# Kernel tuning notes

Measured on AMD Instinct MI355X. Metric: run time of the kernel, lower is better.

The kernel has to match this reference:

```python
import jax, jax.numpy as jnp
import numpy as np

B, N, L = 2, 512, 8
DIM, HEADS, DIM_HEAD, NBRS = 64, 8, 128, 30
INNER = HEADS * DIM_HEAD


def _ln(x, g, b):
    mu = x.mean(-1, keepdims=True)
    v = ((x - mu) ** 2).mean(-1, keepdims=True)
    return (x - mu) * jax.lax.rsqrt(v + 1e-5) * g + b


def _gather_rows(t, idx):
    # t: (n, ...) rows gathered per batch; t (b,n,...), idx (b,i,j) -> (b,i,j,...)
    return jax.vmap(lambda tb, ib: tb[ib])(t, idx)


def _en_layer(h, coors, edges, mask, lp):
    (ln1_g, ln1_b, qkv_w, out_w, out_b, ew1, eb1, ew2, eb2,
     cw1, cb1, cw2, cb2, c_scale, c_comb, ln2_g, ln2_b,
     fw1, fb1, fw2, fb2) = lp
    b, n, _ = h.shape
    x = _ln(h, ln1_g, ln1_b)
    q, k, v = jnp.split(x @ qkv_w, 3, axis=-1)
    q = q.reshape(b, n, HEADS, DIM_HEAD)
    k = k.reshape(b, n, HEADS, DIM_HEAD)
    v = v.reshape(b, n, HEADS, DIM_HEAD)

    rel = coors[:, :, None, :] - coors[:, None, :, :]          # (b,n,n,3)
    dist2 = (rel * rel).sum(-1)                                 # squared dist, same ordering as norm
    pair_ok = mask[:, :, None] & mask[:, None, :]
    ranking = jnp.where(pair_ok, jax.lax.stop_gradient(dist2), 1e10)
    _, idx = jax.lax.top_k(-ranking, NBRS)                      # (b,n,nn) nearest (incl. self)

    kg = _gather_rows(k, idx)                                   # (b,n,nn,h,d)
    vg = _gather_rows(v, idx)
    rel_g = jnp.take_along_axis(rel, idx[..., None], axis=2)    # (b,n,nn,3)
    edg_g = jnp.take_along_axis(edges, idx[..., None], axis=2)  # (b,n,nn,1)
    mask_j = jnp.take_along_axis(jnp.broadcast_to(mask[:, None, :], (b, n, n)), idx, axis=2)
    valid = mask[:, :, None] & mask_j                           # (b,n,nn)

    qk = jnp.einsum('bihd,bijhd->bijh', q, kg) * (DIM_HEAD ** -0.5)
    # edge MLP conditions attention logits on pairwise edge features
    qk = jax.nn.gelu(jnp.concatenate([qk, edg_g], -1) @ ew1 + eb1) @ ew2 + eb2

    # equivariant coordinate update branch
    cw = jax.nn.gelu(jax.nn.gelu(qk) @ cw1 + cb1) @ cw2 + cb2   # (b,n,nn,h)
    cw = jnp.where(valid[..., None], cw, 0.)
    s = (rel_g * rel_g).sum(-1, keepdims=True)
    rel_n = rel_g / jnp.maximum(jnp.sqrt(jnp.where(s == 0., 1., s)), 1e-8) * c_scale
    coors = coors + jnp.einsum('bijh,bijc,h->bic', cw, rel_n, c_comb)

    # node feature attention over the 30 neighbors
    sim = jnp.where(valid[..., None], qk, -1e9)
    attn = jax.nn.softmax(sim, axis=2)
    out = jnp.einsum('bijh,bijhd->bihd', attn, vg).reshape(b, n, INNER)
    h = h + out @ out_w + out_b

    y = _ln(h, ln2_g, ln2_b)
    h = h + jax.nn.gelu(y @ fw1 + fb1) @ fw2 + fb2
    return h, coors


def _forward(mask, feats, coors, edges, fe_w, fe_b, ln1_g, ln1_b, qkv_w, out_w, out_b,
             ew1, eb1, ew2, eb2, cw1, cb1, cw2, cb2, c_scale, c_comb,
             ln2_g, ln2_b, fw1, fb1, fw2, fb2, cls_w, cls_b):
    x = jnp.concatenate([jnp.sin(feats), jnp.cos(feats)], -1)   # (b,n,6)
    h = jax.nn.relu(x @ fe_w + fe_b)                            # (b,n,64)
    lps = (ln1_g, ln1_b, qkv_w, out_w, out_b, ew1, eb1, ew2, eb2,
           cw1, cb1, cw2, cb2, c_scale, c_comb, ln2_g, ln2_b, fw1, fb1, fw2, fb2)

    def step(carry, lp):
        return _en_layer(carry[0], carry[1], edges, mask, lp), None

    (h, _), _ = jax.lax.scan(step, (h, coors), lps)
    return jax.nn.softmax(h @ cls_w + cls_b, axis=2)            # (b,n,20)


def setup_inputs() -> dict:
    key = jax.random.key(0)
    ks = jax.random.split(key, 16)
    r = lambda i, s, sc=0.02: jax.random.normal(ks[i], s, jnp.float32) * sc
    E2 = 2 * (HEADS + 1)
    return dict(
        feats=r(0, (B, N, 3), 1.0),
        coors=r(1, (B, N, 3), 3.0),
        edges=r(2, (B, N, N, 1), 1.0),
        mask=jnp.ones((B, N), dtype=bool),
        fe_w=r(3, (6, DIM)), fe_b=jnp.zeros((DIM,)),
        ln1_g=jnp.ones((L, DIM)), ln1_b=jnp.zeros((L, DIM)),
        qkv_w=r(4, (L, DIM, 3 * INNER)),
        out_w=r(5, (L, INNER, DIM)), out_b=jnp.zeros((L, DIM)),
        ew1=r(6, (L, HEADS + 1, E2), 0.1), eb1=jnp.zeros((L, E2)),
        ew2=r(7, (L, E2, HEADS), 0.1), eb2=jnp.zeros((L, HEADS)),
        cw1=r(8, (L, HEADS, 64), 0.1), cb1=jnp.zeros((L, 64)),
        cw2=r(9, (L, 64, HEADS), 0.1), cb2=jnp.zeros((L, HEADS)),
        c_scale=jnp.ones((L,)),
        c_comb=r(10, (L, HEADS), 0.1),
        ln2_g=jnp.ones((L, DIM)), ln2_b=jnp.zeros((L, DIM)),
        fw1=r(11, (L, DIM, 4 * DIM)), fb1=jnp.zeros((L, 4 * DIM)),
        fw2=r(12, (L, 4 * DIM, DIM)), fb2=jnp.zeros((L, DIM)),
        cls_w=r(13, (DIM, 20)), cls_b=jnp.zeros((20,)),
    )


def reference(feats, coors, edges, mask, fe_w, fe_b, ln1_g, ln1_b, qkv_w, out_w, out_b,
              ew1, eb1, ew2, eb2, cw1, cb1, cw2, cb2, c_scale, c_comb,
              ln2_g, ln2_b, fw1, fb1, fw2, fb2, cls_w, cls_b):
    return _forward(mask, feats, coors, edges, fe_w, fe_b, ln1_g, ln1_b, qkv_w, out_w, out_b,
                    ew1, eb1, ew2, eb2, cw1, cb1, cw2, cb2, c_scale, c_comb,
                    ln2_g, ln2_b, fw1, fb1, fw2, fb2, cls_w, cls_b)
```

## Files before the change

kernel.cpp:

```cpp
#include <hip/hip_runtime.h>
#include <hip/hip_bf16.h>

#define NV    512
#define BN    1024
#define NNB   30
#define DIM   64
#define HEADS 8
#define DH    128
#define INNER 1024

__device__ __forceinline__ float gelu_t(float x){
    float x3 = x*x*x;
    return 0.5f*x*(1.0f + tanhf(0.7978845608028654f*(x + 0.044715f*x3)));
}
__device__ __forceinline__ unsigned short f2bf(float x){
    __hip_bfloat16 h = __float2bfloat16(x);
    return __builtin_bit_cast(unsigned short, h);
}
__device__ __forceinline__ float bflo(unsigned u){ return __uint_as_float(u << 16); }
__device__ __forceinline__ float bfhi(unsigned u){ return __uint_as_float(u & 0xffff0000u); }

__global__ __launch_bounds__(256) void k_head(const float* __restrict__ h,
                                              const float* __restrict__ g,
                                              const float* __restrict__ be,
                                              const float* __restrict__ w,
                                              float* __restrict__ qf,
                                              unsigned short* __restrict__ kvh,
                                              const float* __restrict__ coors,
                                              int* __restrict__ idx,
                                              const float* __restrict__ feats,
                                              const float* __restrict__ fe_w,
                                              const float* __restrict__ fe_b,
                                              float* __restrict__ hout){
    __shared__ float At[64][68];
    __shared__ float Wt[64][132];
    int t = threadIdx.x;
    int wv = t >> 6, lane = t & 63;

    if (blockIdx.x < 384){
        int rt = blockIdx.x / 24, ct = blockIdx.x % 24;
        int row0 = rt*64, col0 = ct*128;

        float gk = g[lane], bk = be[lane];
        if (feats){
            float fb = fe_b[lane];
            float w0 = fe_w[0*DIM+lane], w1 = fe_w[1*DIM+lane], w2 = fe_w[2*DIM+lane];
            float w3 = fe_w[3*DIM+lane], w4 = fe_w[4*DIM+lane], w5 = fe_w[5*DIM+lane];
            #pragma unroll 4
            for (int rr = 0; rr < 16; rr++){
                int r = wv*16 + rr;
                int row = row0 + r;
                float f0 = feats[row*3+0], f1 = feats[row*3+1], f2 = feats[row*3+2];
                float hv = fb;
                hv += sinf(f0)*w0; hv += sinf(f1)*w1; hv += sinf(f2)*w2;
                hv += cosf(f0)*w3; hv += cosf(f1)*w4; hv += cosf(f2)*w5;
                hv = fmaxf(hv, 0.0f);
                if (ct == 0) hout[(size_t)row*DIM + lane] = hv;
                float s = hv;
                #pragma unroll
                for (int m = 32; m >= 1; m >>= 1) s += __shfl_xor(s, m, 64);
                float mu = s*(1.0f/64.0f);
                float d = hv - mu;
                float vv = d*d;
                #pragma unroll
                for (int m = 32; m >= 1; m >>= 1) vv += __shfl_xor(vv, m, 64);
                At[lane][r] = d / sqrtf(vv*(1.0f/64.0f) + 1e-5f) * gk + bk;
            }
        } else {
            #pragma unroll 4
            for (int rr = 0; rr < 16; rr++){
                int r = wv*16 + rr;
                float v = h[(row0+r)*DIM + lane];
                float s = v;
                #pragma unroll
                for (int m = 32; m >= 1; m >>= 1) s += __shfl_xor(s, m, 64);
                float mu = s*(1.0f/64.0f);
                float d = v - mu;
                float vv = d*d;
                #pragma unroll
                for (int m = 32; m >= 1; m >>= 1) vv += __shfl_xor(vv, m, 64);
                At[lane][r] = d / sqrtf(vv*(1.0f/64.0f) + 1e-5f) * gk + bk;
            }
        }
        const float* wg = w + col0;
        #pragma unroll
        for (int i = t*4; i < 64*128; i += 1024){
            int k = i >> 7, c = i & 127;
            *(float4*)&Wt[k][c] = *(const float4*)&wg[k*3072 + c];
        }
        __syncthreads();

        int ty = t >> 4, tx = t & 15;
        float acc[4][8];
        #pragma unroll
        for (int i = 0; i < 4; i++)
            #pragma unroll
            for (int j = 0; j < 8; j++) acc[i][j] = 0.0f;

        #pragma unroll 2
        for (int k = 0; k < 64; k++){
            float4 a  = *(const float4*)&At[k][ty*4];
            float4 w0 = *(const float4*)&Wt[k][tx*4];
            float4 w1 = *(const float4*)&Wt[k][64 + tx*4];
            float av[4]  = {a.x, a.y, a.z, a.w};
            float wv8[8] = {w0.x, w0.y, w0.z, w0.w, w1.x, w1.y, w1.z, w1.w};
            #pragma unroll
            for (int i = 0; i < 4; i++)
                #pragma unroll
                for (int j = 0; j < 8; j++) acc[i][j] += av[i]*wv8[j];
        }

        if (ct < 8){
            #pragma unroll
            for (int i = 0; i < 4; i++){
                int r = row0 + ty*4 + i;
                float* dst = &qf[(size_t)r*INNER + col0];
                *(float4*)&dst[tx*4]      = make_float4(acc[i][0], acc[i][1], acc[i][2], acc[i][3]);
                *(float4*)&dst[64 + tx*4] = make_float4(acc[i][4], acc[i][5], acc[i][6], acc[i][7]);
            }
        } else {
            int kvcol0 = col0 - 1024;
            #pragma unroll
            for (int i = 0; i < 4; i++){
                int r = row0 + ty*4 + i;
                unsigned short* dst = &kvh[(size_t)r*2048 + kvcol0];
                ushort4 p0 = { f2bf(acc[i][0]), f2bf(acc[i][1]), f2bf(acc[i][2]), f2bf(acc[i][3]) };
                ushort4 p1 = { f2bf(acc[i][4]), f2bf(acc[i][5]), f2bf(acc[i][6]), f2bf(acc[i][7]) };
                *(ushort4*)&dst[tx*4]      = p0;
                *(ushort4*)&dst[64 + tx*4] = p1;
            }
        }
    } else {
        int row = (blockIdx.x - 384)*4 + wv;
        int b = row >> 9;
        const float* cbp = coors + (size_t)b*NV*3;
        float cx = coors[row*3+0], cy = coors[row*3+1], cz = coors[row*3+2];
        float d2[8];
        int jb = lane*8;
        #pragma unroll
        for (int u = 0; u < 8; u++){
            float dx = cx - cbp[(jb+u)*3+0];
            float dy = cy - cbp[(jb+u)*3+1];
            float dz = cz - cbp[(jb+u)*3+2];
            d2[u] = dx*dx + dy*dy + dz*dz;
        }
        for (int sel = 0; sel < NNB; sel++){
            float bv = d2[0]; int bu = 0;
            #pragma unroll
            for (int u = 1; u < 8; u++) if (d2[u] < bv){ bv = d2[u]; bu = u; }
            int bj = jb + bu;
            #pragma unroll
            for (int m = 32; m >= 1; m >>= 1){
                float ov = __shfl_xor(bv, m, 64);
                int   oj = __shfl_xor(bj, m, 64);
                if (ov < bv || (ov == bv && oj < bj)){ bv = ov; bj = oj; }
            }
            if (lane == 0) idx[row*NNB + sel] = bj;
            #pragma unroll
            for (int u = 0; u < 8; u++) if (jb + u == bj) d2[u] = 1e30f;
        }
    }
}

__global__ __launch_bounds__(256) void k_layer(const float* __restrict__ qf,
                                               const unsigned short* __restrict__ kvh,
                                               const int*   __restrict__ idx,
                                               const float* __restrict__ cin,
                                               float*       __restrict__ cout,
                                               const float* __restrict__ edges,
                                               float* __restrict__ h,
                                               const float* __restrict__ ew1, const float* __restrict__ eb1,
                                               const float* __restrict__ ew2, const float* __restrict__ eb2,
                                               const float* __restrict__ cw1, const float* __restrict__ cb1,
                                               const float* __restrict__ cw2, const float* __restrict__ cb2,
                                               const float* __restrict__ c_scale, const float* __restrict__ c_comb,
                                               const float* __restrict__ out_w,  const float* __restrict__ out_b,
                                               const float* __restrict__ g2, const float* __restrict__ b2,
                                               const float* __restrict__ fw1, const float* __restrict__ fb1,
                                               const float* __restrict__ fw2, const float* __restrict__ fb2,
                                               const float* __restrict__ cls_w, const float* __restrict__ cls_b,
                                               float* __restrict__ cls_out){
    int row = blockIdx.x;
    int b = row >> 9, i = row & (NV-1);
    int t = threadIdx.x;
    int wave = t >> 6, lane = t & 63;

    __shared__ float qk[NNB][HEADS];
    __shared__ float lg[NNB][HEADS];
    __shared__ float t18[NNB][18];
    __shared__ float t64s[NNB][65];
    __shared__ float cwh[NNB][HEADS];
    __shared__ float attn[NNB][HEADS];
    __shared__ float ej[NNB];
    __shared__ float reln[NNB][3];
    __shared__ float wj[NNB];
    __shared__ int   jid[NNB];
    __shared__ float As[INNER];
    __shared__ float red[256];
    __shared__ float hsr[DIM];
    __shared__ float ys[DIM];
    __shared__ float us[256];

    if (t < NNB) jid[t] = idx[row*NNB + t];
    __syncthreads();

    float qreg[16];
    {
        const float4* qp = (const float4*)&qf[(size_t)row*INNER + lane*16];
        #pragma unroll
        for (int e = 0; e < 4; e++){
            float4 v = qp[e];
            qreg[e*4+0] = v.x; qreg[e*4+1] = v.y; qreg[e*4+2] = v.z; qreg[e*4+3] = v.w;
        }
    }

    if (t < NNB){
        int jj = jid[t];
        ej[t] = edges[(size_t)(b*NV+i)*NV + jj];
        float rx = cin[(b*NV+i)*3+0] - cin[(b*NV+jj)*3+0];
        float ry = cin[(b*NV+i)*3+1] - cin[(b*NV+jj)*3+1];
        float rz = cin[(b*NV+i)*3+2] - cin[(b*NV+jj)*3+2];
        float s = rx*rx + ry*ry + rz*rz;
        float den = fmaxf(sqrtf(s == 0.0f ? 1.0f : s), 1e-8f);
        float cs = c_scale[0];
        reln[t][0] = rx/den*cs;
        reln[t][1] = ry/den*cs;
        reln[t][2] = rz/den*cs;
    }

    int part = lane & 7, hh = lane >> 3;
    #pragma unroll 2
    for (int j = wave; j < NNB; j += 4){
        int jj = jid[j];
        const uint4* kp = (const uint4*)&kvh[(size_t)(b*NV+jj)*2048 + lane*16];
        uint4 u0 = kp[0];
        uint4 u1 = kp[1];
        float acc = qreg[0]*bflo(u0.x) + qreg[1]*bfhi(u0.x)
                  + qreg[2]*bflo(u0.y) + qreg[3]*bfhi(u0.y)
                  + qreg[4]*bflo(u0.z) + qreg[5]*bfhi(u0.z)
                  + qreg[6]*bflo(u0.w) + qreg[7]*bfhi(u0.w);
        acc += qreg[8]*bflo(u1.x)  + qreg[9]*bfhi(u1.x)
             + qreg[10]*bflo(u1.y) + qreg[11]*bfhi(u1.y)
             + qreg[12]*bflo(u1.z) + qreg[13]*bfhi(u1.z)
             + qreg[14]*bflo(u1.w) + qreg[15]*bfhi(u1.w);
        acc += __shfl_xor(acc, 1, 64);
        acc += __shfl_xor(acc, 2, 64);
        acc += __shfl_xor(acc, 4, 64);
        if (part == 0) qk[j][hh] = acc * 0.08838834764831845f;
    }
    __syncthreads();

    for (int id = t; id < NNB*18; id += 256){
        int j = id/18, u = id%18;
        float acc = eb1[u];
        #pragma unroll
        for (int k = 0; k < 8; k++) acc += qk[j][k]*ew1[k*18+u];
        acc += ej[j]*ew1[8*18+u];
        t18[j][u] = gelu_t(acc);
    }
    __syncthreads();
    if (t < NNB*HEADS){
        int j = t/HEADS, h2 = t%HEADS;
        float acc = eb2[h2];
        #pragma unroll
        for (int k = 0; k < 18; k++) acc += t18[j][k]*ew2[k*HEADS+h2];
        lg[j][h2] = acc;
        qk[j][h2] = gelu_t(acc);
    }
    __syncthreads();

    for (int id = t; id < NNB*64; id += 256){
        int j = id/64, u = id%64;
        float acc = cb1[u];
        #pragma unroll
        for (int k = 0; k < 8; k++) acc += qk[j][k]*cw1[k*64+u];
        t64s[j][u] = gelu_t(acc);
    }
    __syncthreads();
    if (t < NNB*HEADS){
        int j = t/HEADS, h2 = t%HEADS;
        float acc = cb2[h2];
        #pragma unroll 8
        for (int k = 0; k < 64; k++) acc += t64s[j][k]*cw2[k*HEADS+h2];
        cwh[j][h2] = acc;
    }
    __syncthreads();

    if (t < NNB){
        float acc = 0.0f;
        #pragma unroll
        for (int h2 = 0; h2 < HEADS; h2++) acc += cwh[t][h2]*c_comb[h2];
        wj[t] = acc;
    }
    if (t >= 64 && t < 128){
        int h2 = (t-64) >> 3, sub = t & 7;
        float v0 = lg[sub][h2];
        float v1 = lg[sub+8][h2];
        float v2 = lg[sub+16][h2];
        float v3 = (sub < 6) ? lg[sub+24][h2] : -1e30f;
        float m = fmaxf(fmaxf(v0,v1), fmaxf(v2,v3));
        m = fmaxf(m, __shfl_xor(m, 1, 64));
        m = fmaxf(m, __shfl_xor(m, 2, 64));
        m = fmaxf(m, __shfl_xor(m, 4, 64));
        float p0 = expf(v0-m), p1 = expf(v1-m), p2 = expf(v2-m);
        float p3 = (sub < 6) ? expf(v3-m) : 0.0f;
        float l = p0+p1+p2+p3;
        l += __shfl_xor(l, 1, 64);
        l += __shfl_xor(l, 2, 64);
        l += __shfl_xor(l, 4, 64);
        float rl = 1.0f/l;
        attn[sub][h2]    = p0*rl;
        attn[sub+8][h2]  = p1*rl;
        attn[sub+16][h2] = p2*rl;
        if (sub < 6) attn[sub+24][h2] = p3*rl;
    }
    __syncthreads();

    if (t < 3){
        float acc = 0.0f;
        for (int j = 0; j < NNB; j++) acc += wj[j]*reln[j][t];
        cout[(b*NV+i)*3+t] = cin[(b*NV+i)*3+t] + acc;
    }

    int hv = t >> 5;
    float ax = 0.f, ay = 0.f, az = 0.f, aw = 0.f;
    for (int j = 0; j < NNB; j++){
        float a = attn[j][hv];
        uint2 v = *(const uint2*)&kvh[(size_t)(b*NV+jid[j])*2048 + 1024 + t*4];
        ax += a*bflo(v.x); ay += a*bfhi(v.x); az += a*bflo(v.y); aw += a*bfhi(v.y);
    }
    *(float4*)&As[t*4] = make_float4(ax, ay, az, aw);
    __syncthreads();

    int d = t & 63, prt = t >> 6;
    {
        float acc = 0.0f;
        const float* as = &As[prt*256];
        const float* wp = &out_w[(size_t)prt*256*DIM + d];
        #pragma unroll 8
        for (int k = 0; k < 256; k++) acc += as[k]*wp[k*DIM];
        red[t] = acc;
    }
    __syncthreads();
    if (t < 64){
        float r = red[t] + red[t+64] + red[t+128] + red[t+192];
        float v = h[(size_t)row*DIM + t] + r + out_b[t];
        hsr[t] = v;
        float s = v;
        #pragma unroll
        for (int m = 32; m >= 1; m >>= 1) s += __shfl_xor(s, m, 64);
        float mu = s*(1.0f/64.0f);
        float dd = v - mu;
        float vv = dd*dd;
        #pragma unroll
        for (int m = 32; m >= 1; m >>= 1) vv += __shfl_xor(vv, m, 64);
        ys[t] = dd / sqrtf(vv*(1.0f/64.0f) + 1e-5f) * g2[t] + b2[t];
    }
    __syncthreads();

    {
        float u = fb1[t];
        #pragma unroll 8
        for (int k = 0; k < 64; k++) u += ys[k]*fw1[k*256 + t];
        us[t] = gelu_t(u);
    }
    __syncthreads();

    {
        float f2 = 0.0f;
        const float* up = &us[prt*64];
        const float* wp2 = &fw2[(size_t)prt*64*DIM + d];
        #pragma unroll 8
        for (int k = 0; k < 64; k++) f2 += up[k]*wp2[k*DIM];
        red[t] = f2;
    }
    __syncthreads();
    if (t < 64){
        float f2 = fb2[t] + red[t] + red[t+64] + red[t+128] + red[t+192];
        float hv = hsr[t] + f2;
        h[(size_t)row*DIM + t] = hv;
        if (cls_out) ys[t] = hv;
    }

    if (cls_out){
        __syncthreads();
        if (t < 20){
            float acc = cls_b[t];
            #pragma unroll 8
            for (int k = 0; k < 64; k++) acc += ys[k]*cls_w[k*20+t];
            red[t] = acc;
        }
        __syncthreads();
        if (t < 20){
            float m = -1e30f;
            for (int c = 0; c < 20; c++) m = fmaxf(m, red[c]);
            float l = 0.0f;
            for (int c = 0; c < 20; c++) l += expf(red[c]-m);
            cls_out[row*20+t] = expf(red[t]-m)/l;
        }
    }
}

extern "C" void kernel_launch(void* const* d_in, const int* in_sizes, int n_in,
                              void* d_out, int out_size, void* d_ws, size_t ws_size,
                              hipStream_t stream) {
    const float* feats = (const float*)d_in[0];
    const float* coors = (const float*)d_in[1];
    const float* edges = (const float*)d_in[2];
    const float* fe_w  = (const float*)d_in[4];
    const float* fe_b  = (const float*)d_in[5];
    const float* ln1_g = (const float*)d_in[6];
    const float* ln1_b = (const float*)d_in[7];
    const float* qkv_w = (const float*)d_in[8];
    const float* out_w = (const float*)d_in[9];
    const float* out_b = (const float*)d_in[10];
    const float* ew1   = (const float*)d_in[11];
    const float* eb1   = (const float*)d_in[12];
    const float* ew2   = (const float*)d_in[13];
    const float* eb2   = (const float*)d_in[14];
    const float* cw1   = (const float*)d_in[15];
    const float* cb1   = (const float*)d_in[16];
    const float* cw2   = (const float*)d_in[17];
    const float* cb2   = (const float*)d_in[18];
    const float* c_scale = (const float*)d_in[19];
    const float* c_comb  = (const float*)d_in[20];
    const float* ln2_g = (const float*)d_in[21];
    const float* ln2_b = (const float*)d_in[22];
    const float* fw1   = (const float*)d_in[23];
    const float* fb1   = (const float*)d_in[24];
    const float* fw2   = (const float*)d_in[25];
    const float* fb2   = (const float*)d_in[26];
    const float* cls_w = (const float*)d_in[27];
    const float* cls_b = (const float*)d_in[28];

    float* ws   = (float*)d_ws;
    float* h    = ws;
    float* cA   = h + BN*DIM;
    float* cB   = cA + BN*3;
    float* qf   = cB + BN*3;
    unsigned short* kvh = (unsigned short*)(qf + (size_t)BN*INNER);
    int*   idx  = (int*)(kvh + (size_t)BN*2048);

    const float* cin = coors;
    float*       cout = cA;
    for (int l = 0; l < 8; l++){
        k_head<<<640, 256, 0, stream>>>(h, ln1_g + l*DIM, ln1_b + l*DIM,
                                        qkv_w + (size_t)l*DIM*3*INNER,
                                        qf, kvh, cin, idx,
                                        (l == 0) ? feats : nullptr, fe_w, fe_b, h);
        k_layer<<<BN, 256, 0, stream>>>(qf, kvh, idx, cin, cout, edges, h,
                                        ew1 + l*9*18,  eb1 + l*18,
                                        ew2 + l*18*8,  eb2 + l*8,
                                        cw1 + l*8*64,  cb1 + l*64,
                                        cw2 + l*64*8,  cb2 + l*8,
                                        c_scale + l,   c_comb + l*8,
                                        out_w + (size_t)l*INNER*DIM, out_b + l*DIM,
                                        ln2_g + l*DIM, ln2_b + l*DIM,
                                        fw1 + (size_t)l*DIM*256, fb1 + l*256,
                                        fw2 + (size_t)l*256*DIM, fb2 + l*64,
                                        cls_w, cls_b,
                                        (l == 7) ? (float*)d_out : nullptr);
        cin = cout;
        cout = (cout == cA) ? cB : cA;
    }
}
```

Baseline: 513.4 us.

## Fuse next-layer LayerNorm into layer kernel and widen layer blocks to 512 threads

The end of k_layer now computes the next layer's LN1 and writes a normalized copy hn, so k_head just loads pre-normalized rows instead of redoing the LN reduction in each of 24 column-tile blocks per row tile. k_layer also moves from 256 to 512 threads per block, splitting the neighbor gather and MLP loops across 8 waves and doing the V aggregation as 2 elements per thread. The tail matmul stages use only half the threads, and launch_bounds(512,8) may force register limits or spills.

```diff
diff --git a/kernel.cpp b/kernel.cpp
--- a/kernel.cpp
+++ b/kernel.cpp
@@ -20,7 +20,7 @@
 __device__ __forceinline__ float bflo(unsigned u){ return __uint_as_float(u << 16); }
 __device__ __forceinline__ float bfhi(unsigned u){ return __uint_as_float(u & 0xffff0000u); }
 
-__global__ __launch_bounds__(256) void k_head(const float* __restrict__ h,
+__global__ __launch_bounds__(256) void k_head(const float* __restrict__ hn,
                                               const float* __restrict__ g,
                                               const float* __restrict__ be,
                                               const float* __restrict__ w,
@@ -41,8 +41,8 @@
         int rt = blockIdx.x / 24, ct = blockIdx.x % 24;
         int row0 = rt*64, col0 = ct*128;
 
-        float gk = g[lane], bk = be[lane];
         if (feats){
+            float gk = g[lane], bk = be[lane];
             float fb = fe_b[lane];
             float w0 = fe_w[0*DIM+lane], w1 = fe_w[1*DIM+lane], w2 = fe_w[2*DIM+lane];
             float w3 = fe_w[3*DIM+lane], w4 = fe_w[4*DIM+lane], w5 = fe_w[5*DIM+lane];
@@ -70,16 +70,7 @@
             #pragma unroll 4
             for (int rr = 0; rr < 16; rr++){
                 int r = wv*16 + rr;
-                float v = h[(row0+r)*DIM + lane];
-                float s = v;
-                #pragma unroll
-                for (int m = 32; m >= 1; m >>= 1) s += __shfl_xor(s, m, 64);
-                float mu = s*(1.0f/64.0f);
-                float d = v - mu;
-                float vv = d*d;
-                #pragma unroll
-                for (int m = 32; m >= 1; m >>= 1) vv += __shfl_xor(vv, m, 64);
-                At[lane][r] = d / sqrtf(vv*(1.0f/64.0f) + 1e-5f) * gk + bk;
+                At[lane][r] = hn[(size_t)(row0+r)*DIM + lane];
             }
         }
         const float* wg = w + col0;
@@ -162,29 +153,26 @@
     }
 }
 
-__global__ __launch_bounds__(256) void k_layer(const float* __restrict__ qf,
-                                               const unsigned short* __restrict__ kvh,
-                                               const int*   __restrict__ idx,
-                                               const float* __restrict__ cin,
-                                               float*       __restrict__ cout,
-                                               const float* __restrict__ edges,
-                                               float* __restrict__ h,
-                                               const float* __restrict__ ew1, const float* __restrict__ eb1,
-                                               const float* __restrict__ ew2, const float* __restrict__ eb2,
-                                               const float* __restrict__ cw1, const float* __restrict__ cb1,
-                                               const float* __restrict__ cw2, const float* __restrict__ cb2,
-                                               const float* __restrict__ c_scale, const float* __restrict__ c_comb,
-                                               const float* __restrict__ out_w,  const float* __restrict__ out_b,
-                                               const float* __restrict__ g2, const float* __restrict__ b2,
-                                               const float* __restrict__ fw1, const float* __restrict__ fb1,
-                                               const float* __restrict__ fw2, const float* __restrict__ fb2,
-                                               const float* __restrict__ cls_w, const float* __restrict__ cls_b,
-                                               float* __restrict__ cls_out){
-    int row = blockIdx.x;
-    int b = row >> 9, i = row & (NV-1);
-    int t = threadIdx.x;
-    int wave = t >> 6, lane = t & 63;
-
+__global__ __launch_bounds__(512, 8) void k_layer(const float* __restrict__ qf,
+                                                const unsigned short* __restrict__ kvh,
+                                                const int*   __restrict__ idx,
+                                                const float* __restrict__ cin,
+                                                float*       __restrict__ cout,
+                                                const float* __restrict__ edges,
+                                                float* __restrict__ h,
+                                                const float* __restrict__ ew1, const float* __restrict__ eb1,
+                                                const float* __restrict__ ew2, const float* __restrict__ eb2,
+                                                const float* __restrict__ cw1, const float* __restrict__ cb1,
+                                                const float* __restrict__ cw2, const float* __restrict__ cb2,
+                                                const float* __restrict__ c_scale, const float* __restrict__ c_comb,
+                                                const float* __restrict__ out_w,  const float* __restrict__ out_b,
+                                                const float* __restrict__ g2, const float* __restrict__ b2,
+                                                const float* __restrict__ fw1, const float* __restrict__ fb1,
+                                                const float* __restrict__ fw2, const float* __restrict__ fb2,
+                                                float* __restrict__ hn,
+                                                const float* __restrict__ g1n, const float* __restrict__ b1n,
+                                                const float* __restrict__ cls_w, const float* __restrict__ cls_b,
+                                                float* __restrict__ cls_out){
     __shared__ float qk[NNB][HEADS];
     __shared__ float lg[NNB][HEADS];
     __shared__ float t18[NNB][18];
@@ -201,6 +189,11 @@
     __shared__ float ys[DIM];
     __shared__ float us[256];
 
+    int t = threadIdx.x;
+    int wv = t >> 6, lane = t & 63;
+    int row = blockIdx.x;
+    int b = row >> 9, i = row & (NV-1);
+
     if (t < NNB) jid[t] = idx[row*NNB + t];
     __syncthreads();
 
@@ -230,7 +223,7 @@
 
     int part = lane & 7, hh = lane >> 3;
     #pragma unroll 2
-    for (int j = wave; j < NNB; j += 4){
+    for (int j = wv; j < NNB; j += 8){
         int jj = jid[j];
         const uint4* kp = (const uint4*)&kvh[(size_t)(b*NV+jj)*2048 + lane*16];
         uint4 u0 = kp[0];
@@ -250,7 +243,7 @@
     }
     __syncthreads();
 
-    for (int id = t; id < NNB*18; id += 256){
+    for (int id = t; id < NNB*18; id += 512){
         int j = id/18, u = id%18;
         float acc = eb1[u];
         #pragma unroll
@@ -269,7 +262,7 @@
     }
     __syncthreads();
 
-    for (int id = t; id < NNB*64; id += 256){
+    for (int id = t; id < NNB*64; id += 512){
         int j = id/64, u = id%64;
         float acc = cb1[u];
         #pragma unroll
@@ -322,18 +315,21 @@
         cout[(b*NV+i)*3+t] = cin[(b*NV+i)*3+t] + acc;
     }
 
-    int hv = t >> 5;
-    float ax = 0.f, ay = 0.f, az = 0.f, aw = 0.f;
-    for (int j = 0; j < NNB; j++){
-        float a = attn[j][hv];
-        uint2 v = *(const uint2*)&kvh[(size_t)(b*NV+jid[j])*2048 + 1024 + t*4];
-        ax += a*bflo(v.x); ay += a*bfhi(v.x); az += a*bflo(v.y); aw += a*bfhi(v.y);
-    }
-    *(float4*)&As[t*4] = make_float4(ax, ay, az, aw);
-    __syncthreads();
-
-    int d = t & 63, prt = t >> 6;
     {
+        int hv = t >> 6;
+        const unsigned short* vb = kvh + (size_t)b*NV*2048 + 1024 + t*2;
+        float ax = 0.f, ay = 0.f;
+        for (int j = 0; j < NNB; j++){
+            float a = attn[j][hv];
+            unsigned v = *(const unsigned*)(vb + (size_t)jid[j]*2048);
+            ax += a*bflo(v); ay += a*bfhi(v);
+        }
+        *(float2*)&As[t*2] = make_float2(ax, ay);
+    }
+    __syncthreads();
+
+    int d = t & 63, prt = (t & 255) >> 6;
+    if (t < 256){
         float acc = 0.0f;
         const float* as = &As[prt*256];
         const float* wp = &out_w[(size_t)prt*256*DIM + d];
@@ -358,7 +354,7 @@
     }
     __syncthreads();
 
-    {
+    if (t < 256){
         float u = fb1[t];
         #pragma unroll 8
         for (int k = 0; k < 64; k++) u += ys[k]*fw1[k*256 + t];
@@ -366,7 +362,7 @@
     }
     __syncthreads();
 
-    {
+    if (t < 256){
         float f2 = 0.0f;
         const float* up = &us[prt*64];
         const float* wp2 = &fw2[(size_t)prt*64*DIM + d];
@@ -379,6 +375,17 @@
         float f2 = fb2[t] + red[t] + red[t+64] + red[t+128] + red[t+192];
         float hv = hsr[t] + f2;
         h[(size_t)row*DIM + t] = hv;
+        if (hn){
+            float s = hv;
+            #pragma unroll
+            for (int m = 32; m >= 1; m >>= 1) s += __shfl_xor(s, m, 64);
+            float mu = s*(1.0f/64.0f);
+            float dd = hv - mu;
+            float vv = dd*dd;
+            #pragma unroll
+            for (int m = 32; m >= 1; m >>= 1) vv += __shfl_xor(vv, m, 64);
+            hn[(size_t)row*DIM + t] = dd / sqrtf(vv*(1.0f/64.0f) + 1e-5f) * g1n[t] + b1n[t];
+        }
         if (cls_out) ys[t] = hv;
     }
 
@@ -435,7 +442,8 @@
 
     float* ws   = (float*)d_ws;
     float* h    = ws;
-    float* cA   = h + BN*DIM;
+    float* hn   = h + BN*DIM;
+    float* cA   = hn + BN*DIM;
     float* cB   = cA + BN*3;
     float* qf   = cB + BN*3;
     unsigned short* kvh = (unsigned short*)(qf + (size_t)BN*INNER);
@@ -444,11 +452,11 @@
     const float* cin = coors;
     float*       cout = cA;
     for (int l = 0; l < 8; l++){
-        k_head<<<640, 256, 0, stream>>>(h, ln1_g + l*DIM, ln1_b + l*DIM,
+        k_head<<<640, 256, 0, stream>>>(hn, ln1_g + l*DIM, ln1_b + l*DIM,
                                         qkv_w + (size_t)l*DIM*3*INNER,
                                         qf, kvh, cin, idx,
                                         (l == 0) ? feats : nullptr, fe_w, fe_b, h);
-        k_layer<<<BN, 256, 0, stream>>>(qf, kvh, idx, cin, cout, edges, h,
+        k_layer<<<BN, 512, 0, stream>>>(qf, kvh, idx, cin, cout, edges, h,
                                         ew1 + l*9*18,  eb1 + l*18,
                                         ew2 + l*18*8,  eb2 + l*8,
                                         cw1 + l*8*64,  cb1 + l*64,
@@ -458,6 +466,9 @@
                                         ln2_g + l*DIM, ln2_b + l*DIM,
                                         fw1 + (size_t)l*DIM*256, fb1 + l*256,
                                         fw2 + (size_t)l*256*DIM, fb2 + l*64,
+                                        (l < 7) ? hn : nullptr,
+                                        ln1_g + (l+1 < 8 ? (l+1)*DIM : 0),
+                                        ln1_b + (l+1 < 8 ? (l+1)*DIM : 0),
                                         cls_w, cls_b,
                                         (l == 7) ? (float*)d_out : nullptr);
         cin = cout;
```

Result: faster. 494.4 us, median of 2 (-3.7%).
